# Kernel optimization log

Hardware: AMD Instinct MI355X
Metric: run time of the kernel (lower is better)

Reference implementation:

```python
import jax, jax.numpy as jnp
import numpy as np

EPS = 1e-5  # torch InstanceNorm3d default


def setup_inputs() -> dict:
    key = jax.random.key(0)
    k1, k2, k3 = jax.random.split(key, 3)
    B, Cin, Cout, T, D, H, W = 1, 32, 64, 2, 48, 48, 48
    x = jax.random.normal(k1, (B, Cin, T, D, H, W), dtype=jnp.float32)
    # Conv4d 'hypercube' kernel: full 3x3x3x3 over (T, D, H, W)
    Wk = jax.random.normal(k2, (Cout, Cin, 3, 3, 3, 3), dtype=jnp.float32) * 0.02
    b = jax.random.normal(k3, (Cout,), dtype=jnp.float32) * 0.02
    return {"x": x, "Wk": Wk, "b": b}


def _forward(x, Wk, b):
    # Per-time-slice InstanceNorm3d (affine=False): normalize over (D,H,W)
    # independently for each (batch, channel, t). Vectorized over t.
    mean = jnp.mean(x, axis=(-3, -2, -1), keepdims=True)
    var = jnp.var(x, axis=(-3, -2, -1), keepdims=True)  # biased, as torch
    h = (x - mean) * jax.lax.rsqrt(var + EPS)
    # Activation (ReLU)
    h = jax.nn.relu(h)
    # Conv4d over spatial dims (T, D, H, W), padding=1, stride 1 + bias.
    dn = jax.lax.ConvDimensionNumbers(
        lhs_spec=(0, 1, 2, 3, 4, 5),  # N, C, T, D, H, W
        rhs_spec=(0, 1, 2, 3, 4, 5),  # O, I, kT, kD, kH, kW
        out_spec=(0, 1, 2, 3, 4, 5),
    )
    out = jax.lax.conv_general_dilated(
        h, Wk,
        window_strides=(1, 1, 1, 1),
        padding=[(1, 1)] * 4,
        dimension_numbers=dn,
    )
    out = out + b[None, :, None, None, None, None]
    # Dropout with drop_rate=0 -> Identity; the per-slice stack is a no-op.
    return out


def reference(x, Wk, b):
    return _forward(x, Wk, b)
```

## Files before the change

### kernel.cpp

```cpp
#include <hip/hip_runtime.h>

namespace {

typedef unsigned short u16;
typedef __attribute__((ext_vector_type(8))) short short8;
typedef __attribute__((ext_vector_type(4))) float f32x4;
typedef __attribute__((ext_vector_type(4))) unsigned int u32x4;

constexpr int kD = 48;
constexpr int kSliceN = kD * kD * kD;
constexpr int kP = 8;

constexpr int SHR1 = 0x111;
constexpr int SHL1 = 0x101;
constexpr int SHL15 = 0x10F;
constexpr int SHR15 = 0x11F;

__device__ inline u16 f2bf(float f) {
  unsigned u = __float_as_uint(f);
  u += 0x7fffu + ((u >> 16) & 1u);
  return (u16)(u >> 16);
}

__device__ inline void gl_lds16(const void* g, void* l) {
  __builtin_amdgcn_global_load_lds(
      (const __attribute__((address_space(1))) unsigned int*)g,
      (__attribute__((address_space(3))) unsigned int*)l, 16, 0, 0);
}

template <int CM>
__device__ inline short8 dpp4(short8 m) {
  u32x4 mu = __builtin_bit_cast(u32x4, m), r;
  #pragma unroll
  for (int j = 0; j < 4; ++j)
    r[j] = (unsigned)__builtin_amdgcn_update_dpp(0, (int)mu[j], CM, 0xf, 0xf, true);
  return __builtin_bit_cast(short8, r);
}
template <int CM, int CP>
__device__ inline short8 dpp4p(short8 m, short8 nb, bool pl) {
  u32x4 mu = __builtin_bit_cast(u32x4, m), nu = __builtin_bit_cast(u32x4, nb), r;
  #pragma unroll
  for (int j = 0; j < 4; ++j) {
    unsigned a = (unsigned)__builtin_amdgcn_update_dpp(0, (int)mu[j], CM, 0xf, 0xf, true);
    unsigned b = (unsigned)__builtin_amdgcn_update_dpp(0, (int)nu[j], CP, 0xf, 0xf, true);
    r[j] = pl ? b : a;
  }
  return __builtin_bit_cast(short8, r);
}

#define MFMA16(A, B, C) __builtin_amdgcn_mfma_f32_16x16x32_bf16((A), (B), (C), 0, 0, 0)

__global__ __launch_bounds__(256) void k_prep(const float* __restrict__ x,
                                              const float* __restrict__ wk,
                                              float* __restrict__ part,
                                              u16* __restrict__ wt) {
  const int tid = threadIdx.x;
  if (blockIdx.x < 64) {
    __shared__ float lw[2592];
    const int co = blockIdx.x;
    const float4* src = reinterpret_cast<const float4*>(wk + (size_t)co * 2592);
    #pragma unroll
    for (int k = 0; k < 3; ++k) {
      const int i = tid + k * 256;
      if (i < 648) ((float4*)lw)[i] = src[i];
    }
    __syncthreads();
    for (int g = tid; g < 324; g += 256) {
      const int tap = g >> 2, kcg = g & 3;
      u32x4 o;
      #pragma unroll
      for (int j = 0; j < 4; ++j) {
        const unsigned lo = f2bf(lw[(kcg * 8 + 2 * j + 0) * 81 + tap]);
        const unsigned hi = f2bf(lw[(kcg * 8 + 2 * j + 1) * 81 + tap]);
        o[j] = lo | (hi << 16);
      }
      *(u32x4*)(wt + (size_t)tap * 2048 + co * 32 + kcg * 8) = o;
    }
    return;
  }
  const int sbid = blockIdx.x - 64;
  const int slice = sbid >> 3;
  const int p = sbid & 7;
  const float4* base = reinterpret_cast<const float4*>(x + (size_t)slice * kSliceN);
  const int per = (kSliceN / 4) / kP;
  const int start = p * per;
  float s = 0.f, sq = 0.f;
  for (int i = start + tid; i < start + per; i += 256) {
    float4 v = base[i];
    s += (v.x + v.y) + (v.z + v.w);
    sq += (v.x * v.x + v.y * v.y) + (v.z * v.z + v.w * v.w);
  }
  #pragma unroll
  for (int off = 32; off > 0; off >>= 1) {
    s += __shfl_down(s, off);
    sq += __shfl_down(sq, off);
  }
  __shared__ float red[2][4];
  const int wave = tid >> 6;
  if ((tid & 63) == 0) { red[0][wave] = s; red[1][wave] = sq; }
  __syncthreads();
  if (tid == 0) {
    s = (red[0][0] + red[0][1]) + (red[0][2] + red[0][3]);
    sq = (red[1][0] + red[1][1]) + (red[1][2] + red[1][3]);
    part[sbid * 2 + 0] = s;
    part[sbid * 2 + 1] = sq;
  }
}

__global__ __launch_bounds__(256) void k_norm(const float* __restrict__ x,
                                              const float* __restrict__ part,
                                              u16* __restrict__ xn) {
  __shared__ u16 ls[6 * 1536];
  __shared__ float sm[32], sr[32];
  const int tid = threadIdx.x;
  const int bid = blockIdx.x;
  const int hs = bid & 7;
  const int dz = (bid >> 3) % 48;
  const int t = bid / 384;
  const int hy0 = hs * 6;

  if (tid < 32) {
    const int slice = tid * 2 + t;
    float s = 0.f, sq = 0.f;
    #pragma unroll
    for (int p = 0; p < kP; ++p) {
      s += part[(slice * kP + p) * 2 + 0];
      sq += part[(slice * kP + p) * 2 + 1];
    }
    const float inv_n = 1.0f / (float)kSliceN;
    const float mean = s * inv_n;
    const float var = sq * inv_n - mean * mean;
    sm[tid] = mean;
    sr[tid] = rsqrtf(var + 1e-5f);
  }
  __syncthreads();

  #pragma unroll
  for (int k = 0; k < 9; ++k) {
    const int F = tid + k * 256;
    const int ci = F / 72;
    const int rem = F - ci * 72;
    const int hy = rem / 12;
    const int wc = rem - hy * 12;
    const float4 v = *reinterpret_cast<const float4*>(
        x + (size_t)(ci * 2 + t) * 110592 + dz * 2304 + (hy0 + hy) * 48 + wc * 4);
    const float mean = sm[ci], rstd = sr[ci];
    const unsigned a0 = f2bf(fmaxf((v.x - mean) * rstd, 0.f));
    const unsigned a1 = f2bf(fmaxf((v.y - mean) * rstd, 0.f));
    const unsigned a2 = f2bf(fmaxf((v.z - mean) * rstd, 0.f));
    const unsigned a3 = f2bf(fmaxf((v.w - mean) * rstd, 0.f));
    uint2 pk;
    pk.x = a0 | (a1 << 16);
    pk.y = a2 | (a3 << 16);
    *reinterpret_cast<uint2*>(ls + hy * 1536 + ci * 48 + wc * 4) = pk;
  }
  __syncthreads();

  const size_t rb = ((size_t)(t * 48 + dz) * 48 + hy0) * 1536;
  #pragma unroll
  for (int k = 0; k < 5; ++k) {
    const int g = tid + k * 256;
    if (g >= 1152) break;
    const int hy = g / 192;
    const int rem = g - hy * 192;
    const int kcg = rem / 48;
    const int w = rem - kcg * 48;
    const u16* base = ls + hy * 1536 + w;
    u32x4 o;
    #pragma unroll
    for (int j = 0; j < 4; ++j) {
      const unsigned lo = base[(kcg * 8 + 2 * j + 0) * 48];
      const unsigned hi = base[(kcg * 8 + 2 * j + 1) * 48];
      o[j] = lo | (hi << 16);
    }
    const int q = w >> 2;
    const int gd = q * 16 + ((kcg ^ (q & 3)) << 2) + (w & 3);
    *(u32x4*)(xn + rb + (size_t)hy * 1536 + gd * 8) = o;
  }
}

__global__ __launch_bounds__(256, 3) void k_conv(const u16* __restrict__ xn,
                                                 const u16* __restrict__ wt,
                                                 const float* __restrict__ bias,
                                                 float* __restrict__ out) {
  __shared__ u16 xs[16 * 1536];
  const int tid = threadIdx.x, wid = tid >> 6, lane = tid & 63;
  const int r15 = lane & 15, kc = lane >> 4;

  const int orig = blockIdx.x;
  const int swz = (orig & 7) * 96 + (orig >> 3);
  const int to = swz & 1;
  const int ht = (swz >> 1) & 7;
  const int dz = swz >> 4;
  const int h0 = ht * 6;

  {
    f32x4 z = {0.f, 0.f, 0.f, 0.f};
    f32x4* p = (f32x4*)xs;
    #pragma unroll
    for (int k = 0; k < 12; ++k) p[tid + k * 256] = z;
  }

  int grano[3];
  #pragma unroll
  for (int wf = 0; wf < 3; ++wf) {
    const int w = wf * 16 + r15, q = w >> 2;
    grano[wf] = (q * 16 + ((kc ^ (q & 3)) << 2) + (w & 3)) << 4;
  }
  const bool pl0 = (r15 == 0), pl15 = (r15 == 15);

  f32x4 acc[6][3];
  #pragma unroll
  for (int m = 0; m < 6; ++m)
    #pragma unroll
    for (int wf = 0; wf < 3; ++wf) acc[m][wf] = (f32x4){0.f, 0.f, 0.f, 0.f};

  __syncthreads();

  for (int dd = 0; dd < 3; ++dd) {
    const int din = dz + dd - 1;
    const bool vd = (din >= 0) && (din < 48);
    if (vd) {
      for (int u = wid; u < 16; u += 4) {
        const int tin = u >> 3, rr = u & 7;
        const int hin = h0 - 1 + rr;
        if (hin < 0 || hin >= 48) continue;
        const u16* src = xn + ((size_t)((tin * 48 + din) * 48 + hin)) * 1536 + lane * 8;
        u16* dstb = xs + u * 1536;
        #pragma unroll
        for (int p = 0; p < 3; ++p) gl_lds16(src + p * 512, dstb + p * 512);
      }
    }
    __syncthreads();
    if (vd) {
      #pragma unroll
      for (int tin = 0; tin < 2; ++tin) {
        const int kt = tin + 1 - to;
        short8 wB[3][3];
        #pragma unroll
        for (int kh = 0; kh < 3; ++kh)
          #pragma unroll
          for (int kw = 0; kw < 3; ++kw)
            wB[kh][kw] = *(const short8*)(wt +
                (size_t)(((kt * 3 + dd) * 3 + kh) * 3 + kw) * 2048 +
                wid * 512 + r15 * 32 + kc * 8);
        #pragma unroll
        for (int r = 0; r < 8; ++r) {
          const char* rb = (const char*)(xs + (tin * 8 + r) * 1536);
          const short8 aC0 = *(const short8*)(rb + grano[0]);
          const short8 aC1 = *(const short8*)(rb + grano[1]);
          const short8 aC2 = *(const short8*)(rb + grano[2]);
          const short8 aL0 = dpp4<SHR1>(aC0);
          const short8 aL1 = dpp4p<SHR1, SHL15>(aC1, aC0, pl0);
          const short8 aL2 = dpp4p<SHR1, SHL15>(aC2, aC1, pl0);
          const short8 aR0 = dpp4p<SHL1, SHR15>(aC0, aC1, pl15);
          const short8 aR1 = dpp4p<SHL1, SHR15>(aC1, aC2, pl15);
          const short8 aR2 = dpp4<SHL1>(aC2);
          #pragma unroll
          for (int kh = 0; kh < 3; ++kh) {
            const int m = r - kh;
            if (m < 0 || m > 5) continue;
            acc[m][0] = MFMA16(wB[kh][0], aL0, acc[m][0]);
            acc[m][0] = MFMA16(wB[kh][1], aC0, acc[m][0]);
            acc[m][0] = MFMA16(wB[kh][2], aR0, acc[m][0]);
            acc[m][1] = MFMA16(wB[kh][0], aL1, acc[m][1]);
            acc[m][1] = MFMA16(wB[kh][1], aC1, acc[m][1]);
            acc[m][1] = MFMA16(wB[kh][2], aR1, acc[m][1]);
            acc[m][2] = MFMA16(wB[kh][0], aL2, acc[m][2]);
            acc[m][2] = MFMA16(wB[kh][1], aC2, acc[m][2]);
            acc[m][2] = MFMA16(wB[kh][2], aR2, acc[m][2]);
          }
        }
      }
    }
    __syncthreads();
  }

  float bv[4];
  #pragma unroll
  for (int j = 0; j < 4; ++j) bv[j] = bias[wid * 16 + kc * 4 + j];
  #pragma unroll
  for (int m = 0; m < 6; ++m) {
    const int hy = h0 + m;
    float* ob = out + (size_t)to * 110592 + (size_t)dz * 2304 + (size_t)hy * 48;
    #pragma unroll
    for (int wf = 0; wf < 3; ++wf) {
      const int w = wf * 16 + r15;
      #pragma unroll
      for (int j = 0; j < 4; ++j) {
        const int co = wid * 16 + kc * 4 + j;
        ob[(size_t)co * 221184 + w] = acc[m][wf][j] + bv[j];
      }
    }
  }
}

}

extern "C" void kernel_launch(void* const* d_in, const int* in_sizes, int n_in,
                              void* d_out, int out_size, void* d_ws, size_t ws_size,
                              hipStream_t stream) {
  const float* x = (const float*)d_in[0];
  const float* wk = (const float*)d_in[1];
  const float* bias = (const float*)d_in[2];
  float* out = (float*)d_out;

  float* part = (float*)d_ws;
  u16* xn = (u16*)((char*)d_ws + 4096);
  u16* wt = xn + 7077888;

  k_prep<<<dim3(576), dim3(256), 0, stream>>>(x, wk, part, wt);
  k_norm<<<dim3(768), dim3(256), 0, stream>>>(x, part, xn);
  k_conv<<<dim3(768), dim3(256), 0, stream>>>(xn, wt, bias, out);
}
```

Measured before the change: 139.5 us.

## Replace DPP lane shifts with padded LDS rows and direct shifted loads

Changes the normalized-activation layout from an XOR-swizzled channel-group order to a plain w-major layout. Each LDS row now carries a zero halo (1600 elements instead of 1536, written at offset 32), so the left, center and right kw taps are read straight from LDS at shifted offsets. This drops the DPP cross-lane shuffles and selects. In exchange there are three LDS reads per wf instead of one, possible bank conflicts from the unswizzled layout, and slightly more shared memory.

```diff
diff --git a/kernel.cpp b/kernel.cpp
--- a/kernel.cpp
+++ b/kernel.cpp
@@ -11,11 +11,6 @@
 constexpr int kSliceN = kD * kD * kD;
 constexpr int kP = 8;
 
-constexpr int SHR1 = 0x111;
-constexpr int SHL1 = 0x101;
-constexpr int SHL15 = 0x10F;
-constexpr int SHR15 = 0x11F;
-
 __device__ inline u16 f2bf(float f) {
   unsigned u = __float_as_uint(f);
   u += 0x7fffu + ((u >> 16) & 1u);
@@ -26,26 +21,6 @@
   __builtin_amdgcn_global_load_lds(
       (const __attribute__((address_space(1))) unsigned int*)g,
       (__attribute__((address_space(3))) unsigned int*)l, 16, 0, 0);
-}
-
-template <int CM>
-__device__ inline short8 dpp4(short8 m) {
-  u32x4 mu = __builtin_bit_cast(u32x4, m), r;
-  #pragma unroll
-  for (int j = 0; j < 4; ++j)
-    r[j] = (unsigned)__builtin_amdgcn_update_dpp(0, (int)mu[j], CM, 0xf, 0xf, true);
-  return __builtin_bit_cast(short8, r);
-}
-template <int CM, int CP>
-__device__ inline short8 dpp4p(short8 m, short8 nb, bool pl) {
-  u32x4 mu = __builtin_bit_cast(u32x4, m), nu = __builtin_bit_cast(u32x4, nb), r;
-  #pragma unroll
-  for (int j = 0; j < 4; ++j) {
-    unsigned a = (unsigned)__builtin_amdgcn_update_dpp(0, (int)mu[j], CM, 0xf, 0xf, true);
-    unsigned b = (unsigned)__builtin_amdgcn_update_dpp(0, (int)nu[j], CP, 0xf, 0xf, true);
-    r[j] = pl ? b : a;
-  }
-  return __builtin_bit_cast(short8, r);
 }
 
 #define MFMA16(A, B, C) __builtin_amdgcn_mfma_f32_16x16x32_bf16((A), (B), (C), 0, 0, 0)
@@ -163,8 +138,8 @@
     if (g >= 1152) break;
     const int hy = g / 192;
     const int rem = g - hy * 192;
-    const int kcg = rem / 48;
-    const int w = rem - kcg * 48;
+    const int w = rem >> 2;
+    const int kcg = rem & 3;
     const u16* base = ls + hy * 1536 + w;
     u32x4 o;
     #pragma unroll
@@ -173,9 +148,7 @@
       const unsigned hi = base[(kcg * 8 + 2 * j + 1) * 48];
       o[j] = lo | (hi << 16);
     }
-    const int q = w >> 2;
-    const int gd = q * 16 + ((kcg ^ (q & 3)) << 2) + (w & 3);
-    *(u32x4*)(xn + rb + (size_t)hy * 1536 + gd * 8) = o;
+    *(u32x4*)(xn + rb + (size_t)hy * 1536 + w * 32 + kcg * 8) = o;
   }
 }
 
@@ -183,7 +156,7 @@
                                                  const u16* __restrict__ wt,
                                                  const float* __restrict__ bias,
                                                  float* __restrict__ out) {
-  __shared__ u16 xs[16 * 1536];
+  __shared__ u16 xs[16 * 1600];
   const int tid = threadIdx.x, wid = tid >> 6, lane = tid & 63;
   const int r15 = lane & 15, kc = lane >> 4;
 
@@ -198,16 +171,13 @@
     f32x4 z = {0.f, 0.f, 0.f, 0.f};
     f32x4* p = (f32x4*)xs;
     #pragma unroll
-    for (int k = 0; k < 12; ++k) p[tid + k * 256] = z;
-  }
-
-  int grano[3];
-  #pragma unroll
-  for (int wf = 0; wf < 3; ++wf) {
-    const int w = wf * 16 + r15, q = w >> 2;
-    grano[wf] = (q * 16 + ((kc ^ (q & 3)) << 2) + (w & 3)) << 4;
-  }
-  const bool pl0 = (r15 == 0), pl15 = (r15 == 15);
+    for (int k = 0; k < 13; ++k) {
+      const int i = tid + k * 256;
+      if (i < 3200) p[i] = z;
+    }
+  }
+
+  const int coff = r15 * 64 + kc * 16;
 
   f32x4 acc[6][3];
   #pragma unroll
@@ -226,7 +196,7 @@
         const int hin = h0 - 1 + rr;
         if (hin < 0 || hin >= 48) continue;
         const u16* src = xn + ((size_t)((tin * 48 + din) * 48 + hin)) * 1536 + lane * 8;
-        u16* dstb = xs + u * 1536;
+        u16* dstb = xs + u * 1600 + 32;
         #pragma unroll
         for (int p = 0; p < 3; ++p) gl_lds16(src + p * 512, dstb + p * 512);
       }
@@ -246,29 +216,20 @@
                 wid * 512 + r15 * 32 + kc * 8);
         #pragma unroll
         for (int r = 0; r < 8; ++r) {
-          const char* rb = (const char*)(xs + (tin * 8 + r) * 1536);
-          const short8 aC0 = *(const short8*)(rb + grano[0]);
-          const short8 aC1 = *(const short8*)(rb + grano[1]);
-          const short8 aC2 = *(const short8*)(rb + grano[2]);
-          const short8 aL0 = dpp4<SHR1>(aC0);
-          const short8 aL1 = dpp4p<SHR1, SHL15>(aC1, aC0, pl0);
-          const short8 aL2 = dpp4p<SHR1, SHL15>(aC2, aC1, pl0);
-          const short8 aR0 = dpp4p<SHL1, SHR15>(aC0, aC1, pl15);
-          const short8 aR1 = dpp4p<SHL1, SHR15>(aC1, aC2, pl15);
-          const short8 aR2 = dpp4<SHL1>(aC2);
+          const char* rb = (const char*)xs + (tin * 8 + r) * 3200;
           #pragma unroll
-          for (int kh = 0; kh < 3; ++kh) {
-            const int m = r - kh;
-            if (m < 0 || m > 5) continue;
-            acc[m][0] = MFMA16(wB[kh][0], aL0, acc[m][0]);
-            acc[m][0] = MFMA16(wB[kh][1], aC0, acc[m][0]);
-            acc[m][0] = MFMA16(wB[kh][2], aR0, acc[m][0]);
-            acc[m][1] = MFMA16(wB[kh][0], aL1, acc[m][1]);
-            acc[m][1] = MFMA16(wB[kh][1], aC1, acc[m][1]);
-            acc[m][1] = MFMA16(wB[kh][2], aR1, acc[m][1]);
-            acc[m][2] = MFMA16(wB[kh][0], aL2, acc[m][2]);
-            acc[m][2] = MFMA16(wB[kh][1], aC2, acc[m][2]);
-            acc[m][2] = MFMA16(wB[kh][2], aR2, acc[m][2]);
+          for (int wf = 0; wf < 3; ++wf) {
+            const short8 A0 = *(const short8*)(rb + wf * 1024 + 0 * 64 + coff);
+            const short8 A1 = *(const short8*)(rb + wf * 1024 + 1 * 64 + coff);
+            const short8 A2 = *(const short8*)(rb + wf * 1024 + 2 * 64 + coff);
+            #pragma unroll
+            for (int kh = 0; kh < 3; ++kh) {
+              const int m = r - kh;
+              if (m < 0 || m > 5) continue;
+              acc[m][wf] = MFMA16(wB[kh][0], A0, acc[m][wf]);
+              acc[m][wf] = MFMA16(wB[kh][1], A1, acc[m][wf]);
+              acc[m][wf] = MFMA16(wB[kh][2], A2, acc[m][wf]);
+            }
           }
         }
       }
```

Measured after the change: 134.4 us. -3.7%, faster.
